# Optimization experiments

Hardware: AMD Instinct MI355X
Metric: run time of the kernel (lower is better)

Reference implementation:

```python
import jax, jax.numpy as jnp
import numpy as np

FORWARD_STEPS = 50
DT = 0.01
G = 9.81
BATCH = 131072


def _rot(psi):
    # batched 6x6 block-rotation matrix R(psi)
    b = psi.shape[0]
    c, s = jnp.cos(psi), jnp.sin(psi)
    R = jnp.zeros((b, 6, 6), dtype=psi.dtype)
    R = R.at[:, 0, 0].set(c).at[:, 0, 2].set(-s)
    R = R.at[:, 1, 1].set(c).at[:, 1, 3].set(-s)
    R = R.at[:, 2, 0].set(s).at[:, 2, 2].set(c)
    R = R.at[:, 3, 1].set(s).at[:, 3, 3].set(c)
    R = R.at[:, 4, 4].set(1.0).at[:, 5, 5].set(1.0)
    return R


def setup_inputs() -> dict:
    key = jax.random.key(0)
    k1, k2, k3, k4, k5 = jax.random.split(key, 5)
    b = BATCH
    # build initial full state [b, 1, 8]: keep body-frame Vx away from 0 (A divides by Vx)
    fs = jnp.zeros((b, 8), dtype=jnp.float32)
    fs = fs.at[:, 0].set(jax.random.normal(k1, (b,)) * 0.1)                     # x
    fs = fs.at[:, 1].set(jax.random.uniform(k2, (b,), minval=0.5, maxval=1.5))  # x_dot
    fs = fs.at[:, 2].set(jax.random.normal(k3, (b,)) * 0.1)                     # y
    fs = fs.at[:, 3].set(jax.random.uniform(k4, (b,), minval=-0.2, maxval=0.2)) # y_dot
    fs = fs.at[:, 4].set(jax.random.uniform(k5, (b,), minval=-0.3, maxval=0.3)) # psi
    fs = fs.at[:, 5].set(jax.random.normal(jax.random.fold_in(key, 10), (b,)) * 0.1)  # psi_dot
    fs = fs.at[:, 6].set(jax.random.normal(jax.random.fold_in(key, 11), (b,)) * 0.1)  # accel cmd
    fs = fs.at[:, 7].set(jax.random.uniform(jax.random.fold_in(key, 12), (b,), minval=-0.2, maxval=0.2))  # steer cmd
    full_states = fs[:, None, :]
    actions = jnp.stack([
        jax.random.normal(jax.random.fold_in(key, 20), (b, FORWARD_STEPS)) * 0.1,
        jax.random.uniform(jax.random.fold_in(key, 21), (b, FORWARD_STEPS), minval=-0.2, maxval=0.2),
    ], axis=-1).astype(jnp.float32)
    m = 0.2
    return {
        "full_states": full_states,
        "actions": actions,
        "m": jnp.float32(m),
        "Caf": jnp.float32(5 * 0.25 * m * G),
        "Car": jnp.float32(5 * 0.25 * m * G),
        "lf": jnp.float32(0.05),
        "lr": jnp.float32(0.05),
        "Iz": jnp.float32((0.1 ** 2 + 0.1 ** 2) / 12.0),
    }


def reference(full_states, actions, m, Caf, Car, lf, lr, Iz):
    bsz = full_states.shape[0]
    dt = jnp.asarray(DT, dtype=full_states.dtype)
    state0 = full_states[:, -1, :6]   # [b,6]
    action0 = full_states[:, -1, 6:]  # [b,2]
    acts = jnp.transpose(actions, (1, 0, 2))  # [T,b,2]

    def step(carry, a_next):
        s, u = carry
        psi = s[:, 4]
        Vx = s[:, 1] * jnp.cos(psi) + s[:, 3] * jnp.sin(psi)
        A = jnp.zeros((bsz, 6, 6), dtype=s.dtype)
        A = A.at[:, 0, 1].set(1.0).at[:, 2, 3].set(1.0).at[:, 4, 5].set(1.0)
        A = A.at[:, 3, 3].set(-(2 * Caf + 2 * Car) / (m * Vx))
        A = A.at[:, 3, 5].set(-Vx - (2 * Caf * lf - 2 * Car * lr) / (m * Vx))
        A = A.at[:, 5, 3].set(-(2 * lf * Caf - 2 * lr * Car) / (Iz * Vx))
        A = A.at[:, 5, 4].set(-(2 * lf ** 2 * Caf + 2 * lr ** 2 * Car) / (Iz * Vx))
        Bm = jnp.zeros((bsz, 6, 2), dtype=s.dtype)
        Bm = Bm.at[:, 1, 0].set(1.0)
        Bm = Bm.at[:, 3, 1].set(2 * Caf / m)
        Bm = Bm.at[:, 5, 1].set(2 * lf * Caf / Iz)
        s_body = jnp.einsum('bij,bj->bi', _rot(-psi), s)
        temp = jnp.einsum('bij,bj->bi', A, s_body) + jnp.einsum('bij,bj->bi', Bm, u)
        pred = s + jnp.einsum('bij,bj->bi', _rot(psi), temp) * dt
        out = jnp.concatenate([pred, a_next], axis=1)  # [b,8]
        return (pred, a_next), out

    _, outs = jax.lax.scan(step, (state0, action0), acts)
    return jnp.transpose(outs, (1, 0, 2))  # [b, forward_steps, 8]
```

## Files before the change

### kernel.cpp

```cpp
#include <hip/hip_runtime.h>

#define DT 0.01f
#define ROW 20

__global__ __launch_bounds__(256) void hybrid_sim_kernel(
    const float* __restrict__ fs,
    const float* __restrict__ actions,
    const float* __restrict__ pm,  const float* __restrict__ pCaf,
    const float* __restrict__ pCar, const float* __restrict__ plf,
    const float* __restrict__ plr, const float* __restrict__ pIz,
    float* __restrict__ out)
{
    __shared__ __align__(16) float lds[4 * 64 * ROW];

    const int tid  = threadIdx.x;
    const int lane = tid & 63;
    const int wv   = tid >> 6;
    const int b    = blockIdx.x * 256 + tid;
    const int b0w  = blockIdx.x * 256 + (wv << 6);

    const float4* fsp = (const float4*)(fs + (size_t)b * 8);
    float4 f0 = fsp[0];
    float4 f1 = fsp[1];
    float s0=f0.x, s1=f0.y, s2=f0.z, s3=f0.w, s4=f1.x, s5=f1.y, u0=f1.z, u1=f1.w;

    float m=*pm, Caf=*pCaf, Car=*pCar, lf=*plf, lr=*plr, Iz=*pIz;
    float k1  = 2.f*(Caf+Car)/m;
    float k2  = 2.f*(Caf*lf-Car*lr)/m;
    float k3  = 2.f*(lf*Caf-lr*Car)/Iz;
    float k4  = 2.f*(lf*lf*Caf+lr*lr*Car)/Iz;
    float b31 = 2.f*Caf/m;
    float b51 = 2.f*lf*Caf/Iz;

    const float4* ap = (const float4*)(actions + (size_t)b * 100);
    float4 abuf[25];
    #pragma unroll
    for (int j = 0; j < 25; ++j) abuf[j] = ap[j];

    float* buf = &lds[wv * 64 * ROW];
    const int rq = lane >> 2;
    const int rm = lane & 3;

    float4 o4[4];

    #pragma unroll
    for (int g = 0; g < 25; ++g) {
        const float4 a4 = abuf[g];
        #pragma unroll
        for (int hh = 0; hh < 2; ++hh) {
            float psi = s4;
            float c  = __cosf(psi);
            float sn = __sinf(psi);
            float Vx  = c*s1 + sn*s3;
            float sb3 = c*s3 - sn*s1;
            float inv = __builtin_amdgcn_rcpf(Vx);
            float t3 = -k1*inv*sb3 + (-Vx - k2*inv)*s5 + b31*u1;
            float t5 = -k3*inv*sb3 - k4*inv*psi + b51*u1;
            float p0 = s0 + DT*(c*Vx - sn*sb3);
            float p2 = s2 + DT*(sn*Vx + c*sb3);
            float p1 = s1 + DT*(c*u0 - sn*t3);
            float p3 = s3 + DT*(sn*u0 + c*t3);
            float p4 = s4 + DT*s5;
            float p5 = s5 + DT*t5;
            float nu0 = hh ? a4.z : a4.x;
            float nu1 = hh ? a4.w : a4.y;
            o4[hh*2 + 0] = make_float4(p0, p1, p2, p3);
            o4[hh*2 + 1] = make_float4(p4, p5, nu0, nu1);
            s0=p0; s1=p1; s2=p2; s3=p3; s4=p4; s5=p5; u0=nu0; u1=nu1;
        }

        #pragma unroll
        for (int j = 0; j < 4; ++j) {
            *(float4*)(buf + lane*ROW + j*4) = o4[j];
        }

        #pragma unroll
        for (int k = 0; k < 4; ++k) {
            const int e = k*16 + rq;
            float4 v = *(const float4*)(buf + e*ROW + rm*4);
            *(float4*)(out + (size_t)(b0w + e)*400 + g*16 + rm*4) = v;
        }
    }
}

extern "C" void kernel_launch(void* const* d_in, const int* in_sizes, int n_in,
                              void* d_out, int out_size, void* d_ws, size_t ws_size,
                              hipStream_t stream) {
    const float* fs      = (const float*)d_in[0];
    const float* actions = (const float*)d_in[1];
    int batch = in_sizes[0] / 8;
    int grid  = batch / 256;
    hybrid_sim_kernel<<<grid, 256, 0, stream>>>(
        fs, actions,
        (const float*)d_in[2], (const float*)d_in[3], (const float*)d_in[4],
        (const float*)d_in[5], (const float*)d_in[6], (const float*)d_in[7],
        (float*)d_out);
}
```

Measured before the change: 309.6 us.

## Replicate each trajectory across four lanes and drop LDS transpose for stores

Each batch element is now simulated redundantly by four threads, and each thread writes one float4 of every 16-float output chunk directly to global memory. This removes the shared-memory staging and transpose that coalesced the output writes. The grid and total compute grow fourfold, and each of the four lanes separately loads the same state and action data.

```diff
diff --git a/kernel.cpp b/kernel.cpp
--- a/kernel.cpp
+++ b/kernel.cpp
@@ -1,7 +1,6 @@
 #include <hip/hip_runtime.h>
 
 #define DT 0.01f
-#define ROW 20
 
 __global__ __launch_bounds__(256) void hybrid_sim_kernel(
     const float* __restrict__ fs,
@@ -11,15 +10,11 @@
     const float* __restrict__ plr, const float* __restrict__ pIz,
     float* __restrict__ out)
 {
-    __shared__ __align__(16) float lds[4 * 64 * ROW];
+    const int tid = threadIdx.x;
+    const int sub = tid & 3;
+    const int e   = blockIdx.x * 64 + (tid >> 2);
 
-    const int tid  = threadIdx.x;
-    const int lane = tid & 63;
-    const int wv   = tid >> 6;
-    const int b    = blockIdx.x * 256 + tid;
-    const int b0w  = blockIdx.x * 256 + (wv << 6);
-
-    const float4* fsp = (const float4*)(fs + (size_t)b * 8);
+    const float4* fsp = (const float4*)(fs + (size_t)e * 8);
     float4 f0 = fsp[0];
     float4 f1 = fsp[1];
     float s0=f0.x, s1=f0.y, s2=f0.z, s3=f0.w, s4=f1.x, s5=f1.y, u0=f1.z, u1=f1.w;
@@ -32,20 +27,17 @@
     float b31 = 2.f*Caf/m;
     float b51 = 2.f*lf*Caf/Iz;
 
-    const float4* ap = (const float4*)(actions + (size_t)b * 100);
+    const float4* ap = (const float4*)(actions + (size_t)e * 100);
     float4 abuf[25];
     #pragma unroll
     for (int j = 0; j < 25; ++j) abuf[j] = ap[j];
 
-    float* buf = &lds[wv * 64 * ROW];
-    const int rq = lane >> 2;
-    const int rm = lane & 3;
-
-    float4 o4[4];
+    float* obase = out + (size_t)e * 400 + sub * 4;
 
     #pragma unroll
     for (int g = 0; g < 25; ++g) {
         const float4 a4 = abuf[g];
+        float4 o4[4];
         #pragma unroll
         for (int hh = 0; hh < 2; ++hh) {
             float psi = s4;
@@ -69,17 +61,11 @@
             s0=p0; s1=p1; s2=p2; s3=p3; s4=p4; s5=p5; u0=nu0; u1=nu1;
         }
 
-        #pragma unroll
-        for (int j = 0; j < 4; ++j) {
-            *(float4*)(buf + lane*ROW + j*4) = o4[j];
-        }
-
-        #pragma unroll
-        for (int k = 0; k < 4; ++k) {
-            const int e = k*16 + rq;
-            float4 v = *(const float4*)(buf + e*ROW + rm*4);
-            *(float4*)(out + (size_t)(b0w + e)*400 + g*16 + rm*4) = v;
-        }
+        float4 v = (sub == 0) ? o4[0]
+                 : (sub == 1) ? o4[1]
+                 : (sub == 2) ? o4[2]
+                 :              o4[3];
+        *(float4*)(obase + g * 16) = v;
     }
 }
 
@@ -89,7 +75,7 @@
     const float* fs      = (const float*)d_in[0];
     const float* actions = (const float*)d_in[1];
     int batch = in_sizes[0] / 8;
-    int grid  = batch / 256;
+    int grid  = (batch * 4) / 256;
     hybrid_sim_kernel<<<grid, 256, 0, stream>>>(
         fs, actions,
         (const float*)d_in[2], (const float*)d_in[3], (const float*)d_in[4],
```

Measured after the change: 404.8 us. +30.7%, slower.
